# Kernel optimization log

Measured on AMD Instinct MI355X. Metric: run time of the kernel, lower is better.

## Reference

```python
import jax, jax.numpy as jnp
import numpy as np

N_NODES = 50000
N_EDGES = 800000
IN_DIM, HID_DIM, OUT_DIM = 128, 128, 256


def _gcn_conv(x, W, b, src, dst, num_nodes):
    # PyG GCNConv: h = D^{-1/2} (A + I) D^{-1/2} X W + b (self-loops already in src/dst)
    h = x @ W  # (N, F_out)
    ones = jnp.ones(src.shape[0], dtype=h.dtype)
    deg = jax.ops.segment_sum(ones, dst, num_segments=num_nodes)
    dinv = jnp.where(deg > 0, jax.lax.rsqrt(deg), 0.0)
    norm = dinv[src] * dinv[dst]  # (E,)
    msg = h[src] * norm[:, None]  # (E, F_out) gather
    out = jax.ops.segment_sum(msg, dst, num_segments=num_nodes)  # scatter-add
    return out + b


def setup_inputs() -> dict:
    key = jax.random.key(0)
    ks = jax.random.split(key, 6)
    x = jax.random.normal(ks[0], (N_NODES, IN_DIM), dtype=jnp.float32)
    edge_index = jax.random.randint(ks[1], (2, N_EDGES), 0, N_NODES, dtype=jnp.int64)
    W1 = jax.random.normal(ks[2], (IN_DIM, HID_DIM), dtype=jnp.float32) / np.sqrt(IN_DIM)
    b1 = jnp.zeros((HID_DIM,), jnp.float32)
    W2 = jax.random.normal(ks[3], (HID_DIM, OUT_DIM), dtype=jnp.float32) / np.sqrt(HID_DIM)
    b2 = jnp.zeros((OUT_DIM,), jnp.float32)
    Wa = jax.random.normal(ks[4], (OUT_DIM, 1), dtype=jnp.float32) / np.sqrt(OUT_DIM)
    ba = jnp.zeros((1,), jnp.float32)
    return {"x": x, "edge_index": edge_index, "W1": W1, "b1": b1, "W2": W2, "b2": b2, "Wa": Wa, "ba": ba}


def reference(x, edge_index, W1, b1, W2, b2, Wa, ba):
    n = x.shape[0]
    loops = jnp.arange(n, dtype=edge_index.dtype)
    src = jnp.concatenate([edge_index[0], loops])
    dst = jnp.concatenate([edge_index[1], loops])
    h = jax.nn.relu(_gcn_conv(x, W1, b1, src, dst, n))
    # dropout is a no-op in eval mode
    node_embeddings = jax.nn.relu(_gcn_conv(h, W2, b2, src, dst, n))
    logits = node_embeddings @ Wa + ba  # (N, 1)
    attn = jax.nn.softmax(logits, axis=0)  # softmax over nodes
    graph_embedding = jnp.sum(node_embeddings * attn, axis=0, keepdims=True)  # (1, OUT_DIM)
    return (node_embeddings, graph_embedding)
```

## Files before the change

### kernel.cpp

```cpp
#include <hip/hip_runtime.h>
#include <hip/hip_fp16.h>
#include <math.h>

typedef __attribute__((ext_vector_type(8))) short bf16x8;
typedef __attribute__((ext_vector_type(4))) float f32x4;

static __device__ __forceinline__ unsigned short f2bf(float x) {
    unsigned u = __float_as_uint(x);
    unsigned r = (u + 0x7FFF + ((u >> 16) & 1)) >> 16;
    return (unsigned short)r;
}
static __device__ __forceinline__ float bf2f(unsigned short h) {
    return __uint_as_float(((unsigned)h) << 16);
}
static __device__ __forceinline__ void addh8(float a[8], uint4 v) {
    float2 f;
    f = __half22float2(*(const __half2*)&v.x); a[0] += f.x; a[1] += f.y;
    f = __half22float2(*(const __half2*)&v.y); a[2] += f.x; a[3] += f.y;
    f = __half22float2(*(const __half2*)&v.z); a[4] += f.x; a[5] += f.y;
    f = __half22float2(*(const __half2*)&v.w); a[6] += f.x; a[7] += f.y;
}


__global__ __launch_bounds__(256) void count_deg_kernel(const int* __restrict__ dst, int E,
                                                        int* __restrict__ deg,
                                                        int* __restrict__ epos) {
    int e = blockIdx.x * 256 + threadIdx.x;
    if (e < E) epos[e] = atomicAdd(&deg[dst[e]], 1);
}

__global__ __launch_bounds__(256) void scan_partial_kernel(const int* __restrict__ deg, int n,
                                                           int* __restrict__ partials) {
    int idx = blockIdx.x * 1024 + threadIdx.x * 4;
    int4 v = make_int4(0, 0, 0, 0);
    if (idx + 3 < n) v = *(const int4*)(deg + idx);
    else {
        if (idx < n) v.x = deg[idx];
        if (idx + 1 < n) v.y = deg[idx + 1];
        if (idx + 2 < n) v.z = deg[idx + 2];
    }
    int s = v.x + v.y + v.z + v.w;
    for (int off = 1; off < 64; off <<= 1) s += __shfl_xor(s, off);
    __shared__ int sm[4];
    int wave = threadIdx.x >> 6;
    if ((threadIdx.x & 63) == 0) sm[wave] = s;
    __syncthreads();
    if (threadIdx.x == 0) partials[blockIdx.x] = sm[0] + sm[1] + sm[2] + sm[3];
}

__global__ __launch_bounds__(64) void scan_offsets_kernel(const int* __restrict__ partials, int nb,
                                                          int* __restrict__ poff,
                                                          int* __restrict__ rowptr, int n) {
    int t = threadIdx.x;
    int v = (t < nb) ? partials[t] : 0;
    int s = v;
    for (int off = 1; off < 64; off <<= 1) {
        int u = __shfl_up(s, off);
        if (t >= off) s += u;
    }
    poff[t] = s - v;
    if (t == 63) rowptr[n] = s;
}

__global__ __launch_bounds__(256) void scan_final_kernel(const int* __restrict__ deg, int n,
                                                         const int* __restrict__ poff,
                                                         int* __restrict__ rowptr) {
    int idx = blockIdx.x * 1024 + threadIdx.x * 4;
    int4 v = make_int4(0, 0, 0, 0);
    if (idx + 3 < n) v = *(const int4*)(deg + idx);
    else {
        if (idx < n) v.x = deg[idx];
        if (idx + 1 < n) v.y = deg[idx + 1];
        if (idx + 2 < n) v.z = deg[idx + 2];
    }
    int tsum = v.x + v.y + v.z + v.w;
    int lane = threadIdx.x & 63, wave = threadIdx.x >> 6;
    int s = tsum;
    for (int off = 1; off < 64; off <<= 1) {
        int u = __shfl_up(s, off);
        if (lane >= off) s += u;
    }
    __shared__ int wsum[4];
    if (lane == 63) wsum[wave] = s;
    __syncthreads();
    int base = poff[blockIdx.x];
    for (int w = 0; w < wave; ++w) base += wsum[w];
    int e0 = base + s - tsum;
    int4 o;
    o.x = e0; o.y = e0 + v.x; o.z = o.y + v.y; o.w = o.z + v.z;
    if (idx + 3 < n) *(int4*)(rowptr + idx) = o;
    else {
        if (idx < n) rowptr[idx] = o.x;
        if (idx + 1 < n) rowptr[idx + 1] = o.y;
        if (idx + 2 < n) rowptr[idx + 2] = o.z;
    }
}

__global__ __launch_bounds__(256) void scatter_kernel(const int* __restrict__ src,
                                                      const int* __restrict__ dst,
                                                      const int* __restrict__ epos, int E,
                                                      const int* __restrict__ rowptr,
                                                      int* __restrict__ csrsrc) {
    int e = blockIdx.x * 256 + threadIdx.x;
    if (e < E) csrsrc[rowptr[dst[e]] + epos[e]] = src[e];
}


__global__ __launch_bounds__(256) void dinv_prescale_kernel(const float* __restrict__ x,
                                                            const int* __restrict__ deg,
                                                            float* __restrict__ dinv,
                                                            __half2* __restrict__ xs16, int n) {
    int node = blockIdx.x * 4 + (threadIdx.x >> 6);
    int lane = threadIdx.x & 63;
    if (node >= n) return;
    float di = rsqrtf((float)(deg[node] + 1));
    if (lane == 0) dinv[node] = di;
    float2 v = *(const float2*)(x + (size_t)node * 128 + (lane << 1));
    xs16[(size_t)node * 64 + lane] = __floats2half2_rn(di * v.x, di * v.y);
}


__global__ __launch_bounds__(256) void wconvert_kernel(const float* __restrict__ W1,
                                                       const float* __restrict__ W2,
                                                       unsigned short* __restrict__ w1h,
                                                       unsigned short* __restrict__ w1l,
                                                       unsigned short* __restrict__ w2h,
                                                       unsigned short* __restrict__ w2l) {
    int i = blockIdx.x * 256 + threadIdx.x;
    if (i < 128 * 128) {
        int nn = i >> 7, k = i & 127;
        float v = W1[k * 128 + nn];
        unsigned short h = f2bf(v);
        w1h[i] = h;
        w1l[i] = f2bf(v - bf2f(h));
    } else if (i < 128 * 128 + 256 * 128) {
        int j = i - 128 * 128;
        int nn = j >> 7, k = j & 127;
        float v = W2[k * 256 + nn];
        unsigned short h = f2bf(v);
        w2h[j] = h;
        w2l[j] = f2bf(v - bf2f(h));
    }
}


__global__ __launch_bounds__(256) void aggregate_kernel(const unsigned short* __restrict__ X16,
                                                        const float* __restrict__ dinv,
                                                        const int* __restrict__ rowptr,
                                                        const int* __restrict__ deg,
                                                        const int* __restrict__ csrsrc,
                                                        unsigned short* __restrict__ outH,
                                                        unsigned short* __restrict__ outL, int n) {
    int node = blockIdx.x * 16 + (threadIdx.x >> 4);
    int sl = threadIdx.x & 15;
    if (node >= n) return;
    const uint4* Xv = (const uint4*)X16;
    float acc[8] = {0.f, 0.f, 0.f, 0.f, 0.f, 0.f, 0.f, 0.f};
    addh8(acc, Xv[(size_t)node * 16 + sl]);
    int e0 = rowptr[node];
    int e1 = e0 + deg[node];
    int e = e0;
    for (; e + 4 <= e1; e += 4) {
        int s0 = csrsrc[e], s1 = csrsrc[e + 1], s2 = csrsrc[e + 2], s3 = csrsrc[e + 3];
        uint4 v0 = Xv[(size_t)s0 * 16 + sl];
        uint4 v1 = Xv[(size_t)s1 * 16 + sl];
        uint4 v2 = Xv[(size_t)s2 * 16 + sl];
        uint4 v3 = Xv[(size_t)s3 * 16 + sl];
        addh8(acc, v0); addh8(acc, v1); addh8(acc, v2); addh8(acc, v3);
    }
    for (; e < e1; ++e) {
        uint4 v = Xv[(size_t)csrsrc[e] * 16 + sl];
        addh8(acc, v);
    }
    float di = dinv[node];
    unsigned short h[8], l[8];
#pragma unroll
    for (int j = 0; j < 8; ++j) {
        float f = di * acc[j];
        h[j] = f2bf(f);
        l[j] = f2bf(f - bf2f(h[j]));
    }
    uint4 hv, lv;
    hv.x = (unsigned)h[0] | ((unsigned)h[1] << 16);
    hv.y = (unsigned)h[2] | ((unsigned)h[3] << 16);
    hv.z = (unsigned)h[4] | ((unsigned)h[5] << 16);
    hv.w = (unsigned)h[6] | ((unsigned)h[7] << 16);
    lv.x = (unsigned)l[0] | ((unsigned)l[1] << 16);
    lv.y = (unsigned)l[2] | ((unsigned)l[3] << 16);
    lv.z = (unsigned)l[4] | ((unsigned)l[5] << 16);
    lv.w = (unsigned)l[6] | ((unsigned)l[7] << 16);
    *(uint4*)(outH + (size_t)node * 128 + sl * 8) = hv;
    *(uint4*)(outL + (size_t)node * 128 + sl * 8) = lv;
}


template <int N, bool SCALE_DINV, bool DO_LOGITS, bool OUT_F16>
__global__ __launch_bounds__(256, 2) void gemm_mfma(const unsigned short* __restrict__ Ah,
                                                    const unsigned short* __restrict__ Al,
                                                    const unsigned short* __restrict__ Bth,
                                                    const unsigned short* __restrict__ Btl,
                                                    const float* __restrict__ bias,
                                                    void* __restrict__ Cout, int M,
                                                    const float* __restrict__ dinv,
                                                    const float* __restrict__ Wa,
                                                    float* __restrict__ logits) {
    __shared__ unsigned short AsH[128 * 64];
    __shared__ unsigned short AsL[128 * 64];
    __shared__ unsigned short BsH[128 * 64];
    __shared__ unsigned short BsL[128 * 64];

    const int t = threadIdx.x;
    const int lane = t & 63;
    const int wave = t >> 6;
    const int wrow = wave >> 1;
    const int wcol = wave & 1;
    const int lq = lane >> 4;
    const int lm = lane & 15;
    const int row0 = blockIdx.x * 128;
    const int col0 = blockIdx.y * 128;

    f32x4 acc[4][4] = {};
    float lacc[4][4] = {};

    for (int kc = 0; kc < 2; ++kc) {
        __syncthreads();
#pragma unroll
        for (int i = 0; i < 4; ++i) {
            int idx = t + i * 256;
            int r = idx >> 3;
            int g = idx & 7;
            int gr = row0 + r;
            uint4 vh = make_uint4(0, 0, 0, 0), vl = make_uint4(0, 0, 0, 0);
            if (gr < M) {
                const size_t go = (size_t)gr * 128 + kc * 64 + g * 8;
                vh = *(const uint4*)(Ah + go);
                vl = *(const uint4*)(Al + go);
            }
            int sg = g ^ (r & 7);
            *(uint4*)(AsH + r * 64 + sg * 8) = vh;
            *(uint4*)(AsL + r * 64 + sg * 8) = vl;
        }
#pragma unroll
        for (int i = 0; i < 4; ++i) {
            int idx = t + i * 256;
            int nn = idx >> 3;
            int g = idx & 7;
            const size_t go = (size_t)(col0 + nn) * 128 + kc * 64 + g * 8;
            int sg = g ^ (nn & 7);
            *(uint4*)(BsH + nn * 64 + sg * 8) = *(const uint4*)(Bth + go);
            *(uint4*)(BsL + nn * 64 + sg * 8) = *(const uint4*)(Btl + go);
        }
        __syncthreads();

#pragma unroll
        for (int ks = 0; ks < 2; ++ks) {
            bf16x8 ah[4], al[4], bh[4], bl[4];
            int gbase = ks * 4 + lq;
#pragma unroll
            for (int rt = 0; rt < 4; ++rt) {
                int ra = wrow * 64 + rt * 16 + lm;
                int off = ra * 64 + (gbase ^ (ra & 7)) * 8;
                ah[rt] = *(const bf16x8*)(AsH + off);
                al[rt] = *(const bf16x8*)(AsL + off);
            }
#pragma unroll
            for (int ct = 0; ct < 4; ++ct) {
                int nb = wcol * 64 + ct * 16 + lm;
                int off = nb * 64 + (gbase ^ (nb & 7)) * 8;
                bh[ct] = *(const bf16x8*)(BsH + off);
                bl[ct] = *(const bf16x8*)(BsL + off);
            }
#pragma unroll
            for (int rt = 0; rt < 4; ++rt)
#pragma unroll
                for (int ct = 0; ct < 4; ++ct) {
                    acc[rt][ct] = __builtin_amdgcn_mfma_f32_16x16x32_bf16(ah[rt], bh[ct], acc[rt][ct], 0, 0, 0);
                    acc[rt][ct] = __builtin_amdgcn_mfma_f32_16x16x32_bf16(al[rt], bh[ct], acc[rt][ct], 0, 0, 0);
                    acc[rt][ct] = __builtin_amdgcn_mfma_f32_16x16x32_bf16(ah[rt], bl[ct], acc[rt][ct], 0, 0, 0);
                }
        }
    }

#pragma unroll
    for (int ct = 0; ct < 4; ++ct) {
        int col = col0 + wcol * 64 + ct * 16 + lm;
        float bc = bias[col];
        float wac = DO_LOGITS ? Wa[col] : 0.f;
#pragma unroll
        for (int rt = 0; rt < 4; ++rt) {
            int rowb = row0 + wrow * 64 + rt * 16 + lq * 4;
#pragma unroll
            for (int reg = 0; reg < 4; ++reg) {
                int gr = rowb + reg;
                if (gr < M) {
                    float o = fmaxf(acc[rt][ct][reg] + bc, 0.f);
                    if (SCALE_DINV) o *= dinv[gr];
                    if (OUT_F16) ((__half*)Cout)[(size_t)gr * N + col] = __float2half(o);
                    else ((float*)Cout)[(size_t)gr * N + col] = o;
                    if (DO_LOGITS) lacc[rt][reg] += o * wac;
                }
            }
        }
    }

    if (DO_LOGITS) {
#pragma unroll
        for (int rt = 0; rt < 4; ++rt)
#pragma unroll
            for (int reg = 0; reg < 4; ++reg) {
                float s = lacc[rt][reg];
                s += __shfl_xor(s, 1);
                s += __shfl_xor(s, 2);
                s += __shfl_xor(s, 4);
                s += __shfl_xor(s, 8);
                int gr = row0 + wrow * 64 + rt * 16 + lq * 4 + reg;
                if (lm == 0 && gr < M) atomicAdd(&logits[gr], s);
            }
    }
}


__global__ __launch_bounds__(256) void maxsum_kernel(const float* __restrict__ logits, int n,
                                                     float2* __restrict__ part) {
    float m = -INFINITY, s = 0.f;
    for (int i = blockIdx.x * 256 + threadIdx.x; i < n; i += gridDim.x * 256) {
        float v = logits[i];
        if (v > m) { s = s * expf(m - v) + 1.f; m = v; }
        else s += expf(v - m);
    }
    __shared__ float sm[256], ss[256];
    sm[threadIdx.x] = m; ss[threadIdx.x] = s;
    __syncthreads();
    for (int off = 128; off > 0; off >>= 1) {
        if (threadIdx.x < off) {
            float m1 = sm[threadIdx.x], s1 = ss[threadIdx.x];
            float m2 = sm[threadIdx.x + off], s2 = ss[threadIdx.x + off];
            float M = fmaxf(m1, m2);
            sm[threadIdx.x] = M;
            ss[threadIdx.x] = s1 * expf(m1 - M) + s2 * expf(m2 - M);
        }
        __syncthreads();
    }
    if (threadIdx.x == 0) part[blockIdx.x] = make_float2(sm[0], ss[0]);
}

__global__ __launch_bounds__(64) void merge_kernel(const float2* __restrict__ part,
                                                   float* __restrict__ gms) {
    __shared__ float sm[64], ss[64];
    float2 p = part[threadIdx.x];
    sm[threadIdx.x] = p.x; ss[threadIdx.x] = p.y;
    __syncthreads();
    for (int off = 32; off > 0; off >>= 1) {
        if (threadIdx.x < off) {
            float m1 = sm[threadIdx.x], s1 = ss[threadIdx.x];
            float m2 = sm[threadIdx.x + off], s2 = ss[threadIdx.x + off];
            float M = fmaxf(m1, m2);
            sm[threadIdx.x] = M;
            ss[threadIdx.x] = s1 * expf(m1 - M) + s2 * expf(m2 - M);
        }
        __syncthreads();
    }
    if (threadIdx.x == 0) { gms[0] = sm[0]; gms[1] = ss[0]; }
}

__global__ __launch_bounds__(256) void weighted_sum_kernel(const float* __restrict__ emb,
                                                           const float* __restrict__ logits,
                                                           const float* __restrict__ gms,
                                                           float* __restrict__ gpart, int n) {
    float g = gms[0];
    int wave = threadIdx.x >> 6;
    int lane = threadIdx.x & 63;
    int stride = gridDim.x * 4;
    float4 acc = make_float4(0.f, 0.f, 0.f, 0.f);
#pragma unroll 2
    for (int r = blockIdx.x * 4 + wave; r < n; r += stride) {
        float w = expf(logits[r] - g);
        float4 v = *(const float4*)(emb + (size_t)r * 256 + (lane << 2));
        acc.x += w * v.x; acc.y += w * v.y; acc.z += w * v.z; acc.w += w * v.w;
    }
    __shared__ float4 sm[256];
    sm[threadIdx.x] = acc;
    __syncthreads();
    if (wave == 0) {
        float4 a = sm[lane], b = sm[64 + lane], c = sm[128 + lane], d = sm[192 + lane];
        float4 s;
        s.x = (a.x + b.x) + (c.x + d.x);
        s.y = (a.y + b.y) + (c.y + d.y);
        s.z = (a.z + b.z) + (c.z + d.z);
        s.w = (a.w + b.w) + (c.w + d.w);
        *(float4*)(gpart + (size_t)blockIdx.x * 256 + (lane << 2)) = s;
    }
}

__global__ __launch_bounds__(256) void reduce_gpart_kernel(const float* __restrict__ gpart,
                                                           float* __restrict__ outTail, int nb) {
    int rows = nb / gridDim.x;
    int r0 = blockIdx.x * rows;
    float s = 0.f;
    for (int r = r0; r < r0 + rows; ++r) s += gpart[(size_t)r * 256 + threadIdx.x];
    atomicAdd(&outTail[threadIdx.x], s);
}

__global__ __launch_bounds__(256) void normalize_kernel(float* __restrict__ outTail,
                                                        const float* __restrict__ gms) {
    outTail[threadIdx.x] = outTail[threadIdx.x] / gms[1];
}


extern "C" void kernel_launch(void* const* d_in, const int* in_sizes, int n_in,
                              void* d_out, int out_size, void* d_ws, size_t ws_size,
                              hipStream_t stream) {
    const float* x  = (const float*)d_in[0];
    const int* ei   = (const int*)d_in[1];
    const float* W1 = (const float*)d_in[2];
    const float* b1 = (const float*)d_in[3];
    const float* W2 = (const float*)d_in[4];
    const float* b2 = (const float*)d_in[5];
    const float* Wa = (const float*)d_in[6];
    float* out = (float*)d_out;

    const int n = in_sizes[0] / 128;
    const int E = in_sizes[1] / 2;
    const int* srcA = ei;
    const int* dstA = ei + E;
    const int nb = (n + 1023) / 1024;
    const int WS_BLOCKS = 1024;

    unsigned short* xs16 = (unsigned short*)d_ws;
    unsigned short* aggH = xs16 + (size_t)n * 128;
    unsigned short* aggL = aggH + (size_t)n * 128;
    unsigned short* w1h  = aggL + (size_t)n * 128;
    unsigned short* w1l  = w1h + 128 * 128;
    unsigned short* w2h  = w1l + 128 * 128;
    unsigned short* w2l  = w2h + 256 * 128;
    float* dinv   = (float*)(w2l + 256 * 128);
    float* logits = dinv + n;
    float2* part  = (float2*)(logits + n);
    float* gms    = (float*)(part + 64);
    float* gpart  = gms + 2;
    int* deg      = (int*)(gpart + WS_BLOCKS * 256);
    int* rowptr   = deg + n;
    int* partials = rowptr + n + 1;
    int* poff     = partials + 64;
    int* epos     = poff + 64;
    int* csrsrc   = epos + E;

    hipMemsetAsync(deg, 0, sizeof(int) * (size_t)n, stream);
    hipMemsetAsync(logits, 0, sizeof(float) * (size_t)n, stream);
    hipMemsetAsync(out + (size_t)n * 256, 0, sizeof(float) * 256, stream);

    count_deg_kernel<<<(E + 255) / 256, 256, 0, stream>>>(dstA, E, deg, epos);
    scan_partial_kernel<<<nb, 256, 0, stream>>>(deg, n, partials);
    scan_offsets_kernel<<<1, 64, 0, stream>>>(partials, nb, poff, rowptr, n);
    scan_final_kernel<<<nb, 256, 0, stream>>>(deg, n, poff, rowptr);
    scatter_kernel<<<(E + 255) / 256, 256, 0, stream>>>(srcA, dstA, epos, E, rowptr, csrsrc);
    dinv_prescale_kernel<<<(n + 3) / 4, 256, 0, stream>>>(x, deg, dinv, (__half2*)xs16, n);
    wconvert_kernel<<<(128 * 128 + 256 * 128 + 255) / 256, 256, 0, stream>>>(W1, W2, w1h, w1l, w2h, w2l);

    int aggBlocks = (n + 15) / 16;
    int gemmRows = (n + 127) / 128;

    aggregate_kernel<<<aggBlocks, 256, 0, stream>>>(xs16, dinv, rowptr, deg, csrsrc, aggH, aggL, n);
    gemm_mfma<128, true, false, true><<<dim3(gemmRows, 1), 256, 0, stream>>>(
        aggH, aggL, w1h, w1l, b1, xs16, n, dinv, nullptr, nullptr);
    aggregate_kernel<<<aggBlocks, 256, 0, stream>>>(xs16, dinv, rowptr, deg, csrsrc, aggH, aggL, n);
    gemm_mfma<256, false, true, false><<<dim3(gemmRows, 2), 256, 0, stream>>>(
        aggH, aggL, w2h, w2l, b2, out, n, nullptr, Wa, logits);

    maxsum_kernel<<<64, 256, 0, stream>>>(logits, n, part);
    merge_kernel<<<1, 64, 0, stream>>>(part, gms);
    weighted_sum_kernel<<<WS_BLOCKS, 256, 0, stream>>>(out, logits, gms, gpart, n);
    reduce_gpart_kernel<<<32, 256, 0, stream>>>(gpart, out + (size_t)n * 256, WS_BLOCKS);
    normalize_kernel<<<1, 256, 0, stream>>>(out + (size_t)n * 256, gms);
}
```

Before: 311.4 us.

## Load MFMA operands directly from global memory, dropping LDS staging

The split-bf16 GEMM no longer stages A and B tiles through shared memory with swizzling and barriers. Each wave now loads its MFMA fragments straight from global memory, with out-of-range rows clamped to the last row, and launch bounds are raised to 3 blocks per CU. The aim is to remove LDS traffic and synchronisation and raise occupancy. The cost is duplicated global and L2 loads across waves, since each A and B fragment is fetched by two waves instead of once per block, plus less coalesced 16-byte row loads.

```diff
diff --git a/kernel.cpp b/kernel.cpp
--- a/kernel.cpp
+++ b/kernel.cpp
@@ -195,7 +195,7 @@
 
 
 template <int N, bool SCALE_DINV, bool DO_LOGITS, bool OUT_F16>
-__global__ __launch_bounds__(256, 2) void gemm_mfma(const unsigned short* __restrict__ Ah,
+__global__ __launch_bounds__(256, 3) void gemm_mfma(const unsigned short* __restrict__ Ah,
                                                     const unsigned short* __restrict__ Al,
                                                     const unsigned short* __restrict__ Bth,
                                                     const unsigned short* __restrict__ Btl,
@@ -204,11 +204,6 @@
                                                     const float* __restrict__ dinv,
                                                     const float* __restrict__ Wa,
                                                     float* __restrict__ logits) {
-    __shared__ unsigned short AsH[128 * 64];
-    __shared__ unsigned short AsL[128 * 64];
-    __shared__ unsigned short BsH[128 * 64];
-    __shared__ unsigned short BsL[128 * 64];
-
     const int t = threadIdx.x;
     const int lane = t & 63;
     const int wave = t >> 6;
@@ -219,66 +214,41 @@
     const int row0 = blockIdx.x * 128;
     const int col0 = blockIdx.y * 128;
 
+    int ar[4];
+#pragma unroll
+    for (int rt = 0; rt < 4; ++rt) {
+        int r = row0 + wrow * 64 + rt * 16 + lm;
+        ar[rt] = (r < M) ? r : (M - 1);
+    }
+    const int cb = col0 + wcol * 64 + lm;
+
     f32x4 acc[4][4] = {};
     float lacc[4][4] = {};
 
-    for (int kc = 0; kc < 2; ++kc) {
-        __syncthreads();
-#pragma unroll
-        for (int i = 0; i < 4; ++i) {
-            int idx = t + i * 256;
-            int r = idx >> 3;
-            int g = idx & 7;
-            int gr = row0 + r;
-            uint4 vh = make_uint4(0, 0, 0, 0), vl = make_uint4(0, 0, 0, 0);
-            if (gr < M) {
-                const size_t go = (size_t)gr * 128 + kc * 64 + g * 8;
-                vh = *(const uint4*)(Ah + go);
-                vl = *(const uint4*)(Al + go);
+#pragma unroll
+    for (int kq = 0; kq < 4; ++kq) {
+        const int ko = kq * 32 + lq * 8;
+        bf16x8 a_h[4], a_l[4], b_h[4], b_l[4];
+#pragma unroll
+        for (int rt = 0; rt < 4; ++rt) {
+            const size_t o = (size_t)ar[rt] * 128 + ko;
+            a_h[rt] = *(const bf16x8*)(Ah + o);
+            a_l[rt] = *(const bf16x8*)(Al + o);
+        }
+#pragma unroll
+        for (int ct = 0; ct < 4; ++ct) {
+            const size_t o = (size_t)(cb + ct * 16) * 128 + ko;
+            b_h[ct] = *(const bf16x8*)(Bth + o);
+            b_l[ct] = *(const bf16x8*)(Btl + o);
+        }
+#pragma unroll
+        for (int rt = 0; rt < 4; ++rt)
+#pragma unroll
+            for (int ct = 0; ct < 4; ++ct) {
+                acc[rt][ct] = __builtin_amdgcn_mfma_f32_16x16x32_bf16(a_h[rt], b_h[ct], acc[rt][ct], 0, 0, 0);
+                acc[rt][ct] = __builtin_amdgcn_mfma_f32_16x16x32_bf16(a_l[rt], b_h[ct], acc[rt][ct], 0, 0, 0);
+                acc[rt][ct] = __builtin_amdgcn_mfma_f32_16x16x32_bf16(a_h[rt], b_l[ct], acc[rt][ct], 0, 0, 0);
             }
-            int sg = g ^ (r & 7);
-            *(uint4*)(AsH + r * 64 + sg * 8) = vh;
-            *(uint4*)(AsL + r * 64 + sg * 8) = vl;
-        }
-#pragma unroll
-        for (int i = 0; i < 4; ++i) {
-            int idx = t + i * 256;
-            int nn = idx >> 3;
-            int g = idx & 7;
-            const size_t go = (size_t)(col0 + nn) * 128 + kc * 64 + g * 8;
-            int sg = g ^ (nn & 7);
-            *(uint4*)(BsH + nn * 64 + sg * 8) = *(const uint4*)(Bth + go);
-            *(uint4*)(BsL + nn * 64 + sg * 8) = *(const uint4*)(Btl + go);
-        }
-        __syncthreads();
-
-#pragma unroll
-        for (int ks = 0; ks < 2; ++ks) {
-            bf16x8 ah[4], al[4], bh[4], bl[4];
-            int gbase = ks * 4 + lq;
-#pragma unroll
-            for (int rt = 0; rt < 4; ++rt) {
-                int ra = wrow * 64 + rt * 16 + lm;
-                int off = ra * 64 + (gbase ^ (ra & 7)) * 8;
-                ah[rt] = *(const bf16x8*)(AsH + off);
-                al[rt] = *(const bf16x8*)(AsL + off);
-            }
-#pragma unroll
-            for (int ct = 0; ct < 4; ++ct) {
-                int nb = wcol * 64 + ct * 16 + lm;
-                int off = nb * 64 + (gbase ^ (nb & 7)) * 8;
-                bh[ct] = *(const bf16x8*)(BsH + off);
-                bl[ct] = *(const bf16x8*)(BsL + off);
-            }
-#pragma unroll
-            for (int rt = 0; rt < 4; ++rt)
-#pragma unroll
-                for (int ct = 0; ct < 4; ++ct) {
-                    acc[rt][ct] = __builtin_amdgcn_mfma_f32_16x16x32_bf16(ah[rt], bh[ct], acc[rt][ct], 0, 0, 0);
-                    acc[rt][ct] = __builtin_amdgcn_mfma_f32_16x16x32_bf16(al[rt], bh[ct], acc[rt][ct], 0, 0, 0);
-                    acc[rt][ct] = __builtin_amdgcn_mfma_f32_16x16x32_bf16(ah[rt], bl[ct], acc[rt][ct], 0, 0, 0);
-                }
-        }
     }
 
 #pragma unroll
```

Result: slower. 333.7 us (+7.2%).

## Load GEMM tiles directly into LDS with global_load_lds using pre-swizzled layouts

Applied to the files above, without the earlier changes.

The GEMM tile loads now use the global_load_lds builtin, so data goes from global memory straight into shared memory instead of through registers. To keep the XOR bank swizzle that the shared-memory reads expect, the weight-conversion and aggregation kernels now write their bf16 hi/lo outputs already swizzled in global memory. This cuts register pressure and load/store instructions in the GEMM staging. It drops the row bounds check and zero-fill for the last partial tile, so it relies on padded buffers or tolerates reads past M.

```diff
diff --git a/kernel.cpp b/kernel.cpp
--- a/kernel.cpp
+++ b/kernel.cpp
@@ -19,6 +19,11 @@
     f = __half22float2(*(const __half2*)&v.y); a[2] += f.x; a[3] += f.y;
     f = __half22float2(*(const __half2*)&v.z); a[4] += f.x; a[5] += f.y;
     f = __half22float2(*(const __half2*)&v.w); a[6] += f.x; a[7] += f.y;
+}
+static __device__ __forceinline__ void gll16(const unsigned short* g, unsigned short* l) {
+    __builtin_amdgcn_global_load_lds(
+        (const __attribute__((address_space(1))) unsigned int*)(const void*)g,
+        (__attribute__((address_space(3))) unsigned int*)(void*)l, 16, 0, 0);
 }
 
 
@@ -131,15 +136,17 @@
         int nn = i >> 7, k = i & 127;
         float v = W1[k * 128 + nn];
         unsigned short h = f2bf(v);
-        w1h[i] = h;
-        w1l[i] = f2bf(v - bf2f(h));
+        int kp = (k & 64) + ((((k >> 3) & 7) ^ (nn & 7)) << 3) + (k & 7);
+        w1h[nn * 128 + kp] = h;
+        w1l[nn * 128 + kp] = f2bf(v - bf2f(h));
     } else if (i < 128 * 128 + 256 * 128) {
         int j = i - 128 * 128;
         int nn = j >> 7, k = j & 127;
         float v = W2[k * 256 + nn];
         unsigned short h = f2bf(v);
-        w2h[j] = h;
-        w2l[j] = f2bf(v - bf2f(h));
+        int kp = (k & 64) + ((((k >> 3) & 7) ^ (nn & 7)) << 3) + (k & 7);
+        w2h[nn * 128 + kp] = h;
+        w2l[nn * 128 + kp] = f2bf(v - bf2f(h));
     }
 }
 
@@ -189,8 +196,9 @@
     lv.y = (unsigned)l[2] | ((unsigned)l[3] << 16);
     lv.z = (unsigned)l[4] | ((unsigned)l[5] << 16);
     lv.w = (unsigned)l[6] | ((unsigned)l[7] << 16);
-    *(uint4*)(outH + (size_t)node * 128 + sl * 8) = hv;
-    *(uint4*)(outL + (size_t)node * 128 + sl * 8) = lv;
+    int pos = ((sl & 8) | ((sl & 7) ^ (node & 7))) * 8;
+    *(uint4*)(outH + (size_t)node * 128 + pos) = hv;
+    *(uint4*)(outL + (size_t)node * 128 + pos) = lv;
 }
 
 
@@ -219,36 +227,24 @@
     const int row0 = blockIdx.x * 128;
     const int col0 = blockIdx.y * 128;
 
+    const int lr = lane >> 3;
+    const int p8 = (lane & 7) * 8;
+
     f32x4 acc[4][4] = {};
     float lacc[4][4] = {};
 
     for (int kc = 0; kc < 2; ++kc) {
         __syncthreads();
 #pragma unroll
-        for (int i = 0; i < 4; ++i) {
-            int idx = t + i * 256;
-            int r = idx >> 3;
-            int g = idx & 7;
-            int gr = row0 + r;
-            uint4 vh = make_uint4(0, 0, 0, 0), vl = make_uint4(0, 0, 0, 0);
-            if (gr < M) {
-                const size_t go = (size_t)gr * 128 + kc * 64 + g * 8;
-                vh = *(const uint4*)(Ah + go);
-                vl = *(const uint4*)(Al + go);
-            }
-            int sg = g ^ (r & 7);
-            *(uint4*)(AsH + r * 64 + sg * 8) = vh;
-            *(uint4*)(AsL + r * 64 + sg * 8) = vl;
-        }
-#pragma unroll
-        for (int i = 0; i < 4; ++i) {
-            int idx = t + i * 256;
-            int nn = idx >> 3;
-            int g = idx & 7;
-            const size_t go = (size_t)(col0 + nn) * 128 + kc * 64 + g * 8;
-            int sg = g ^ (nn & 7);
-            *(uint4*)(BsH + nn * 64 + sg * 8) = *(const uint4*)(Bth + go);
-            *(uint4*)(BsL + nn * 64 + sg * 8) = *(const uint4*)(Btl + go);
+        for (int j = 0; j < 4; ++j) {
+            int seg = wave * 4 + j;
+            int r = seg * 8 + lr;
+            size_t goA = (size_t)(row0 + r) * 128 + kc * 64 + p8;
+            size_t goB = (size_t)(col0 + r) * 128 + kc * 64 + p8;
+            gll16(Ah + goA, AsH + seg * 512);
+            gll16(Al + goA, AsL + seg * 512);
+            gll16(Bth + goB, BsH + seg * 512);
+            gll16(Btl + goB, BsL + seg * 512);
         }
         __syncthreads();
 
```

Result: no change. 309.2 us (-0.7%).
